# Performance work log

Hardware: AMD Instinct MI355X
Metric: run time of the kernel (lower is better)

The kernel has to match this reference:

```python
import jax, jax.numpy as jnp
import numpy as np

B, S, D = 4, 2048, 1024
H, DK, DV = 16, 64, 64
LN_EPS = 1e-5


def setup_inputs() -> dict:
    key = jax.random.key(0)
    ks = jax.random.split(key, 6)
    x = jax.random.normal(ks[0], (B, S, D), dtype=jnp.float32)
    # causal mask: True = masked position (j > i), broadcast over batch
    causal = jnp.triu(jnp.ones((S, S), dtype=bool), k=1)
    attention_mask = jnp.broadcast_to(causal, (B, S, S))
    scale = 1.0 / np.sqrt(D)
    w_q = jax.random.normal(ks[1], (D, H * DK), dtype=jnp.float32) * scale
    w_k = jax.random.normal(ks[2], (D, H * DK), dtype=jnp.float32) * scale
    w_v = jax.random.normal(ks[3], (D, H * DV), dtype=jnp.float32) * scale
    w_fc = jax.random.normal(ks[4], (H * DV, D), dtype=jnp.float32) * (1.0 / np.sqrt(H * DV))
    ln_gamma = jnp.ones((D,), dtype=jnp.float32)
    ln_beta = jnp.zeros((D,), dtype=jnp.float32)
    return {"x": x, "attention_mask": attention_mask, "w_q": w_q, "w_k": w_k,
            "w_v": w_v, "w_fc": w_fc, "ln_gamma": ln_gamma, "ln_beta": ln_beta}


def _layernorm(y, gamma, beta):
    mu = jnp.mean(y, axis=-1, keepdims=True)
    var = jnp.mean(jnp.square(y - mu), axis=-1, keepdims=True)
    return (y - mu) * jax.lax.rsqrt(var + LN_EPS) * gamma + beta


def reference(x, attention_mask, w_q, w_k, w_v, w_fc, ln_gamma, ln_beta):
    b, s, _ = x.shape
    # projections -> [b, h, s, dk/dv]
    q = (x @ w_q).reshape(b, s, H, DK).transpose(0, 2, 1, 3)
    k = (x @ w_k).reshape(b, s, H, DK).transpose(0, 2, 1, 3)
    v = (x @ w_v).reshape(b, s, H, DV).transpose(0, 2, 1, 3)
    # scaled dot-product attention with mask (True -> -1e9)
    scores = jnp.einsum('bhqd,bhkd->bhqk', q, k) / np.sqrt(DK)
    scores = jnp.where(attention_mask[:, None, :, :], jnp.float32(-1e9), scores)
    attn = jax.nn.softmax(scores, axis=-1)
    context = jnp.einsum('bhqk,bhkd->bhqd', attn, v)
    context = context.transpose(0, 2, 1, 3).reshape(b, s, H * DV)
    output = context @ w_fc
    out = _layernorm(output + x, ln_gamma, ln_beta)
    return out, attn
```

## Files before the change

### kernel.cpp

```cpp
#include <hip/hip_runtime.h>
#include <stdint.h>

#define S_LEN 2048
#define NHEAD 16

typedef short short8 __attribute__((ext_vector_type(8)));
typedef float f32x4 __attribute__((ext_vector_type(4)));
typedef unsigned short u16;

typedef __attribute__((address_space(1))) uint32_t AS1u32;
typedef __attribute__((address_space(3))) uint32_t AS3u32;

#define MFMA16(a, b, c) __builtin_amdgcn_mfma_f32_16x16x32_bf16((a), (b), (c), 0, 0, 0)

__device__ __forceinline__ void gload16(const void* g, void* l) {
  __builtin_amdgcn_global_load_lds((AS1u32*)g, (AS3u32*)l, 16, 0, 0);
}

__device__ __forceinline__ u16 f2bf(float f) {
  union { float f; uint32_t u; } c; c.f = f;
  return (u16)((c.u + 0x7fffu + ((c.u >> 16) & 1u)) >> 16);
}

__global__ __launch_bounds__(256) void prep_kernel(
    const float* __restrict__ x, u16* __restrict__ xb,
    const float* __restrict__ w0, const float* __restrict__ w1,
    const float* __restrict__ w2, const float* __restrict__ w3,
    u16* __restrict__ qkvT, u16* __restrict__ fcT) {
  __shared__ float t[32][33];
  int bid = blockIdx.x;
  if (bid < 8192) {
    size_t i = ((size_t)bid * 256 + threadIdx.x) * 4;
    f32x4 v = *(const f32x4*)(x + i);
    union { u16 h[4]; uint2 d; } o;
    o.h[0] = f2bf(v[0]); o.h[1] = f2bf(v[1]); o.h[2] = f2bf(v[2]); o.h[3] = f2bf(v[3]);
    *(uint2*)(xb + i) = o.d;
    return;
  }
  int r = bid - 8192;
  int z = r >> 10; r &= 1023;
  int bx = r & 31, by = r >> 5;
  const float* w = (z == 0) ? w0 : (z == 1) ? w1 : (z == 2) ? w2 : w3;
  u16* o = (z == 3) ? fcT : qkvT + (size_t)z * 1048576;
  float scale = (z == 0) ? 0.125f : 1.0f;
  int n0 = bx * 32, k0 = by * 32;
  int tx = threadIdx.x & 31, ty = threadIdx.x >> 5;
#pragma unroll
  for (int i = 0; i < 4; ++i) {
    int k = ty * 4 + i;
    t[k][tx] = w[(size_t)(k0 + k) * 1024 + n0 + tx];
  }
  __syncthreads();
#pragma unroll
  for (int i = 0; i < 4; ++i) {
    int n = ty * 4 + i;
    o[(size_t)(n0 + n) * 1024 + k0 + tx] = f2bf(t[tx][n] * scale);
  }
}

__device__ __forceinline__ void gemm_stage(const char* Ab, const char* Bb, u16* As, u16* Bs,
                                           int m0, int n0, int kbyte, int tid) {
#pragma unroll
  for (int i = 0; i < 2; ++i) {
    int cid = i * 256 + tid;
    int row = cid >> 2, c = cid & 3;
    int off = kbyte + ((c ^ ((row >> 1) & 3)) << 4);
    gload16(Ab + (size_t)(m0 + row) * 2048 + off, (char*)As + i * 4096 + (tid & ~63) * 16);
    gload16(Bb + (size_t)(n0 + row) * 2048 + off, (char*)Bs + i * 4096 + (tid & ~63) * 16);
  }
}

__global__ __launch_bounds__(256) void gemm_bt_kernel(
    const u16* __restrict__ A, const u16* __restrict__ BT,
    void* __restrict__ out, void* __restrict__ outv, int mode) {
  __shared__ u16 sh[128 * 128];
  u16* As = sh;
  u16* Bs = sh + 4096;
  const int tid = threadIdx.x;
  const int lane = tid & 63, wv = tid >> 6;
  const int l15 = lane & 15, h16 = lane >> 4;
  const int wr = wv >> 1, wc = wv & 1;
  const int m0 = blockIdx.x * 128, n0 = blockIdx.y * 128;
  const char* Ab = (const char*)A;
  const char* Bb = (const char*)BT;

  f32x4 acc[4][4];
#pragma unroll
  for (int i = 0; i < 4; ++i)
#pragma unroll
    for (int j = 0; j < 4; ++j) acc[i][j] = (f32x4){0.f, 0.f, 0.f, 0.f};

  gemm_stage(Ab, Bb, As, Bs, m0, n0, 0, tid);
  for (int kt = 0; kt < 32; ++kt) {
    __syncthreads();
    short8 a[4], b[4];
#pragma unroll
    for (int mf = 0; mf < 4; ++mf) {
      int row = wr * 64 + mf * 16 + l15;
      a[mf] = *(const short8*)((const char*)As + row * 64 + ((h16 ^ ((row >> 1) & 3)) << 4));
    }
#pragma unroll
    for (int nf = 0; nf < 4; ++nf) {
      int row = wc * 64 + nf * 16 + l15;
      b[nf] = *(const short8*)((const char*)Bs + row * 64 + ((h16 ^ ((row >> 1) & 3)) << 4));
    }
#pragma unroll
    for (int mf = 0; mf < 4; ++mf)
#pragma unroll
      for (int nf = 0; nf < 4; ++nf)
        acc[mf][nf] = MFMA16(a[mf], b[nf], acc[mf][nf]);
    __syncthreads();
    if (kt + 1 < 32) gemm_stage(Ab, Bb, As, Bs, m0, n0, (kt + 1) * 64, tid);
  }

  if (mode == 0 && n0 < 2048) {
    u16* o = (u16*)out;
#pragma unroll
    for (int mf = 0; mf < 4; ++mf)
#pragma unroll
      for (int nf = 0; nf < 4; ++nf)
#pragma unroll
        for (int r = 0; r < 4; ++r) {
          int row = wr * 64 + mf * 16 + 4 * h16 + r;
          int col = wc * 64 + nf * 16 + l15;
          *(u16*)((char*)sh + row * 256 + (((col >> 3) ^ (row & 7)) << 4) + (col & 7) * 2) =
              f2bf(acc[mf][nf][r]);
        }
    __syncthreads();
    int row = tid >> 1, hf = tid & 1;
    int m = m0 + row;
    int bb = m >> 11, s = m & 2047;
    int n_base = n0 + hf * 64;
    int z = n_base >> 10, nn = n_base & 1023, hh = nn >> 6;
    u16* dst = o + (size_t)z * 8388608 + (((size_t)(bb * NHEAD + hh) * S_LEN + s) << 6);
#pragma unroll
    for (int i = 0; i < 8; ++i) {
      int ch = hf * 8 + i;
      short8 v = *(const short8*)((const char*)sh + row * 256 + ((ch ^ (row & 7)) << 4));
      *(short8*)(dst + i * 8) = v;
    }
  } else if (mode == 0) {
    u16* o = (u16*)outv;
#pragma unroll
    for (int mf = 0; mf < 4; ++mf)
#pragma unroll
      for (int nf = 0; nf < 4; ++nf)
#pragma unroll
        for (int r = 0; r < 4; ++r) {
          int row = wr * 64 + mf * 16 + 4 * h16 + r;
          int col = wc * 64 + nf * 16 + l15;
          *(u16*)((char*)sh + col * 256 + (((row >> 3) ^ (col & 7)) << 4) + (row & 7) * 2) =
              f2bf(acc[mf][nf][r]);
        }
    __syncthreads();
    int col = tid >> 1, half = tid & 1;
    int bb = m0 >> 11, s0 = (m0 & 2047) + half * 64;
    int nn = n0 - 2048 + col;
    int hh = nn >> 6, dv = nn & 63;
    u16* dst = o + ((size_t)(bb * NHEAD + hh) * 64 + dv) * S_LEN + s0;
    const char* base = (const char*)sh + col * 256;
#pragma unroll
    for (int i = 0; i < 8; ++i) {
      int ch = (half * 8 + i) ^ (col & 7);
      *(short8*)(dst + i * 8) = *(const short8*)(base + (ch << 4));
    }
  } else {
    float* o = (float*)out;
#pragma unroll
    for (int mf = 0; mf < 4; ++mf)
#pragma unroll
      for (int nf = 0; nf < 4; ++nf)
#pragma unroll
        for (int r = 0; r < 4; ++r) {
          int m = m0 + wr * 64 + mf * 16 + 4 * h16 + r;
          int n = n0 + wc * 64 + nf * 16 + l15;
          o[(size_t)m * 1024 + n] = acc[mf][nf][r];
        }
  }
}

__device__ __forceinline__ void stage_qk(const char* base, int row0, u16* dst, int tid) {
#pragma unroll
  for (int i = 0; i < 2; ++i) {
    int cid = i * 512 + tid;
    int row = cid >> 3, c = cid & 7;
    gload16(base + (size_t)(row0 + row) * 128 + ((c ^ (row & 7)) << 4),
            (char*)dst + i * 8192 + (tid & ~63) * 16);
  }
}
__device__ __forceinline__ void stage_v(const char* Vb, int kv0, u16* dst, int tid) {
#pragma unroll
  for (int i = 0; i < 2; ++i) {
    int cid = i * 512 + tid;
    int row = cid >> 4, c = cid & 15;
    gload16(Vb + (size_t)row * 4096 + (size_t)kv0 * 2 + ((c ^ (row & 7)) << 4),
            (char*)dst + i * 8192 + (tid & ~63) * 16);
  }
}

__device__ __forceinline__ void qk_tile(const char* Kc, const short8* qf,
                                        f32x4* sc, int l15, int h16) {
#pragma unroll
  for (int nf = 0; nf < 8; ++nf) sc[nf] = (f32x4){0.f, 0.f, 0.f, 0.f};
#pragma unroll
  for (int ks = 0; ks < 2; ++ks)
#pragma unroll
    for (int nf = 0; nf < 8; ++nf) {
      int row = nf * 16 + l15;
      short8 kb = *(const short8*)(Kc + row * 128 + (((ks * 4 + h16) ^ (row & 7)) << 4));
      sc[nf] = MFMA16(qf[ks], kb, sc[nf]);
    }
}

__device__ __forceinline__ void attn_one(
    const u16* __restrict__ Q, const u16* __restrict__ K, const u16* __restrict__ VT,
    float* __restrict__ attn, u16* __restrict__ ctx, int qt, int bh, int tid,
    u16 (*Ks)[128 * 64], u16* Vs, u16* Ps) {
  const int lane = tid & 63, wv = tid >> 6;
  const int l15 = lane & 15, h16 = lane >> 4;
  const int w16 = wv * 16;
  const int q0 = qt * 128;
  const char* Qb = (const char*)(Q + (size_t)bh * S_LEN * 64);
  const char* Kb = (const char*)(K + (size_t)bh * S_LEN * 64);
  const char* Vb = (const char*)(VT + (size_t)bh * 64 * S_LEN);
  float* attb = attn + (size_t)bh * S_LEN * S_LEN;

  stage_qk(Qb, q0, Ps, tid);
  stage_qk(Kb, q0, Ks[0], tid);
  __syncthreads();
  short8 qf[2];
  {
    int row = w16 + l15;
    qf[0] = *(const short8*)((const char*)Ps + row * 128 + ((h16 ^ (row & 7)) << 4));
    qf[1] = *(const short8*)((const char*)Ps + row * 128 + (((4 + h16) ^ (row & 7)) << 4));
  }
  __syncthreads();

  float lsum[4] = {0.f, 0.f, 0.f, 0.f};
  int cur = 0;
  for (int t = qt; t >= 0; --t) {
    if (t > 0) stage_qk(Kb, (t - 1) * 128, Ks[cur ^ 1], tid);
    f32x4 sc[8];
    qk_tile((const char*)Ks[cur], qf, sc, l15, h16);
    if (t == qt) {
#pragma unroll
      for (int nf = 0; nf < 8; ++nf)
#pragma unroll
        for (int r = 0; r < 4; ++r)
          if (nf * 16 + l15 > w16 + 4 * h16 + r) sc[nf][r] = -1e30f;
    }
#pragma unroll
    for (int nf = 0; nf < 8; ++nf)
#pragma unroll
      for (int r = 0; r < 4; ++r) lsum[r] += __expf(sc[nf][r]);
    __syncthreads();
    cur ^= 1;
  }
  cur ^= 1;
  f32x4 ri;
#pragma unroll
  for (int r = 0; r < 4; ++r) {
    float v = lsum[r];
    v += __shfl_xor(v, 1);
    v += __shfl_xor(v, 2);
    v += __shfl_xor(v, 4);
    v += __shfl_xor(v, 8);
    ri[r] = 1.0f / v;
  }

  f32x4 cacc[4];
#pragma unroll
  for (int nf = 0; nf < 4; ++nf) cacc[nf] = (f32x4){0.f, 0.f, 0.f, 0.f};

  for (int t = 0; t <= qt; ++t) {
    const int kv0 = t * 128;
    stage_v(Vb, kv0, Vs, tid);
    f32x4 sc[8];
    qk_tile((const char*)Ks[cur], qf, sc, l15, h16);
    if (t == qt) {
#pragma unroll
      for (int nf = 0; nf < 8; ++nf)
#pragma unroll
        for (int r = 0; r < 4; ++r)
          if (nf * 16 + l15 > w16 + 4 * h16 + r) sc[nf][r] = -1e30f;
    }
    {
      float* arow = attb + (size_t)(q0 + w16 + 4 * h16) * S_LEN + kv0 + l15;
#pragma unroll
      for (int nf = 0; nf < 8; ++nf)
#pragma unroll
        for (int r = 0; r < 4; ++r) {
          float p = __expf(sc[nf][r]) * ri[r];
          int rowL = w16 + 4 * h16 + r;
          int chunk = 2 * nf + (l15 >> 3);
          *(u16*)((char*)Ps + rowL * 256 + ((chunk ^ (rowL & 7)) << 4) + (l15 & 7) * 2) = f2bf(p);
          arow[(size_t)r * S_LEN + nf * 16] = p;
        }
    }
    __syncthreads();
    if (t < qt) stage_qk(Kb, kv0 + 128, Ks[cur ^ 1], tid);
#pragma unroll
    for (int ks = 0; ks < 4; ++ks) {
      int rowP = w16 + l15;
      short8 pa = *(const short8*)((const char*)Ps + rowP * 256 + (((ks * 4 + h16) ^ (rowP & 7)) << 4));
#pragma unroll
      for (int nf = 0; nf < 4; ++nf) {
        int rowV = nf * 16 + l15;
        short8 vbf = *(const short8*)((const char*)Vs + rowV * 256 + (((ks * 4 + h16) ^ (rowV & 7)) << 4));
        cacc[nf] = MFMA16(pa, vbf, cacc[nf]);
      }
    }
    __syncthreads();
    cur ^= 1;
  }

  for (int kvt = qt + 1; kvt < 16; ++kvt) {
    const int kv0 = kvt * 128;
    int row = tid >> 2, sub = tid & 3;
    float* arow = attb + (size_t)(q0 + row) * S_LEN + kv0;
    f32x4 z = {0.f, 0.f, 0.f, 0.f};
#pragma unroll
    for (int c8 = 0; c8 < 4; ++c8) {
      int chunk = sub + 4 * c8;
      *(f32x4*)(arow + chunk * 8) = z;
      *(f32x4*)(arow + chunk * 8 + 4) = z;
    }
  }

  {
    int b = bh >> 4, hh = bh & 15;
#pragma unroll
    for (int nf = 0; nf < 4; ++nf)
#pragma unroll
      for (int r = 0; r < 4; ++r) {
        int qrow = q0 + w16 + 4 * h16 + r;
        ctx[((size_t)b * S_LEN + qrow) * 1024 + hh * 64 + nf * 16 + l15] = f2bf(cacc[nf][r]);
      }
  }
}

__global__ __launch_bounds__(512) void attn2_kernel(
    const u16* __restrict__ Q, const u16* __restrict__ K, const u16* __restrict__ VT,
    float* __restrict__ attn, u16* __restrict__ ctx) {
  __shared__ u16 Ks[2][128 * 64];
  __shared__ u16 Vs[64 * 128];
  __shared__ u16 Ps[128 * 128];
  const int tid = threadIdx.x;
  const int w = blockIdx.x;
  const int bx = (w >> 3) & 7;
  const int bh = (w & 7) + ((w >> 6) << 3);
  attn_one(Q, K, VT, attn, ctx, 15 - bx, bh, tid, Ks, Vs, Ps);
  attn_one(Q, K, VT, attn, ctx, bx, bh, tid, Ks, Vs, Ps);
}

__global__ __launch_bounds__(256) void ln_kernel(float* __restrict__ io,
                                                 const float* __restrict__ x,
                                                 const float* __restrict__ gamma,
                                                 const float* __restrict__ beta) {
  int row = blockIdx.x, tid = threadIdx.x;
  size_t base = (size_t)row * 1024 + tid * 4;
  f32x4 p = *(const f32x4*)(io + base);
  f32x4 xv = *(const f32x4*)(x + base);
  f32x4 y;
  float s1 = 0.f, s2 = 0.f;
#pragma unroll
  for (int j = 0; j < 4; ++j) {
    y[j] = p[j] + xv[j];
    s1 += y[j];
    s2 += y[j] * y[j];
  }
#pragma unroll
  for (int off = 1; off <= 32; off <<= 1) {
    s1 += __shfl_xor(s1, off);
    s2 += __shfl_xor(s2, off);
  }
  __shared__ float r1[4], r2[4];
  int w = tid >> 6;
  if ((tid & 63) == 0) { r1[w] = s1; r2[w] = s2; }
  __syncthreads();
  float S1 = r1[0] + r1[1] + r1[2] + r1[3];
  float S2 = r2[0] + r2[1] + r2[2] + r2[3];
  float mu = S1 * (1.f / 1024.f);
  float var = S2 * (1.f / 1024.f) - mu * mu;
  float rs = rsqrtf(var + 1e-5f);
  f32x4 g = *(const f32x4*)(gamma + tid * 4);
  f32x4 bt = *(const f32x4*)(beta + tid * 4);
  f32x4 o;
#pragma unroll
  for (int j = 0; j < 4; ++j) o[j] = (y[j] - mu) * rs * g[j] + bt[j];
  *(f32x4*)(io + base) = o;
}

extern "C" void kernel_launch(void* const* d_in, const int* in_sizes, int n_in,
                              void* d_out, int out_size, void* d_ws, size_t ws_size,
                              hipStream_t stream) {
  (void)in_sizes; (void)n_in; (void)out_size; (void)ws_size;
  const float* x = (const float*)d_in[0];
  const float* wq = (const float*)d_in[2];
  const float* wk = (const float*)d_in[3];
  const float* wv = (const float*)d_in[4];
  const float* wfc = (const float*)d_in[5];
  const float* gamma = (const float*)d_in[6];
  const float* beta = (const float*)d_in[7];

  char* ws = (char*)d_ws;
  u16* xb = (u16*)ws;
  u16* wqkvT = (u16*)(ws + (16u << 20));
  u16* wfcT = (u16*)(ws + (22u << 20));
  u16* qkb = (u16*)(ws + (24u << 20));
  u16* qb = qkb;
  u16* kb = qkb + (size_t)8388608;
  u16* vT = (u16*)(ws + (56u << 20));
  u16* ctx = xb;

  float* outp = (float*)d_out;
  float* attnp = outp + (size_t)4 * 2048 * 1024;

  prep_kernel<<<12288, 256, 0, stream>>>(x, xb, wq, wk, wv, wfc, wqkvT, wfcT);
  gemm_bt_kernel<<<dim3(64, 24), 256, 0, stream>>>(xb, wqkvT, qkb, vT, 0);
  attn2_kernel<<<512, 512, 0, stream>>>(qb, kb, vT, attnp, ctx);
  gemm_bt_kernel<<<dim3(64, 8), 256, 0, stream>>>(ctx, wfcT, outp, nullptr, 1);
  ln_kernel<<<8192, 256, 0, stream>>>(outp, x, gamma, beta);
}
```

Baseline: 473.1 us.

## Rewrite attention as per-wave 16-row strips with direct global loads and shuffles

Replaces the block-cooperative 128x128 attention tile, which staged K and V in shared memory behind block-wide barriers, with independent per-wavefront 16-query-row strips. Each wave loads Q, K and V fragments straight from global memory and computes 16x16 score tiles with swapped MFMA operands. It rebuilds the P operand for the PV product through cross-lane shuffles instead of an LDS round trip, and uses a small LDS transpose only to coalesce the fp32 attention stores. The intent is to remove __syncthreads stalls, improve causal load balance and raise occupancy. The cost is that K and V are no longer shared across waves, so global/L2 traffic rises, and the smaller MFMA tiles reuse less data.

```diff
diff --git a/kernel.cpp b/kernel.cpp
--- a/kernel.cpp
+++ b/kernel.cpp
@@ -179,178 +179,155 @@
   }
 }
 
-__device__ __forceinline__ void stage_qk(const char* base, int row0, u16* dst, int tid) {
-#pragma unroll
-  for (int i = 0; i < 2; ++i) {
-    int cid = i * 512 + tid;
-    int row = cid >> 3, c = cid & 7;
-    gload16(base + (size_t)(row0 + row) * 128 + ((c ^ (row & 7)) << 4),
-            (char*)dst + i * 8192 + (tid & ~63) * 16);
-  }
-}
-__device__ __forceinline__ void stage_v(const char* Vb, int kv0, u16* dst, int tid) {
-#pragma unroll
-  for (int i = 0; i < 2; ++i) {
-    int cid = i * 512 + tid;
-    int row = cid >> 4, c = cid & 15;
-    gload16(Vb + (size_t)row * 4096 + (size_t)kv0 * 2 + ((c ^ (row & 7)) << 4),
-            (char*)dst + i * 8192 + (tid & ~63) * 16);
-  }
-}
-
-__device__ __forceinline__ void qk_tile(const char* Kc, const short8* qf,
-                                        f32x4* sc, int l15, int h16) {
-#pragma unroll
-  for (int nf = 0; nf < 8; ++nf) sc[nf] = (f32x4){0.f, 0.f, 0.f, 0.f};
-#pragma unroll
-  for (int ks = 0; ks < 2; ++ks)
-#pragma unroll
-    for (int nf = 0; nf < 8; ++nf) {
-      int row = nf * 16 + l15;
-      short8 kb = *(const short8*)(Kc + row * 128 + (((ks * 4 + h16) ^ (row & 7)) << 4));
-      sc[nf] = MFMA16(qf[ks], kb, sc[nf]);
-    }
-}
-
-__device__ __forceinline__ void attn_one(
-    const u16* __restrict__ Q, const u16* __restrict__ K, const u16* __restrict__ VT,
-    float* __restrict__ attn, u16* __restrict__ ctx, int qt, int bh, int tid,
-    u16 (*Ks)[128 * 64], u16* Vs, u16* Ps) {
-  const int lane = tid & 63, wv = tid >> 6;
+__device__ __forceinline__ void attn3_strip(
+    const u16* __restrict__ Qb, const u16* __restrict__ Kb, const u16* __restrict__ Vb,
+    float* __restrict__ attb, u16* __restrict__ ctx, int bh, int s, int lane,
+    float (*myP)[20]) {
   const int l15 = lane & 15, h16 = lane >> 4;
-  const int w16 = wv * 16;
-  const int q0 = qt * 128;
-  const char* Qb = (const char*)(Q + (size_t)bh * S_LEN * 64);
-  const char* Kb = (const char*)(K + (size_t)bh * S_LEN * 64);
-  const char* Vb = (const char*)(VT + (size_t)bh * 64 * S_LEN);
-  float* attb = attn + (size_t)bh * S_LEN * S_LEN;
-
-  stage_qk(Qb, q0, Ps, tid);
-  stage_qk(Kb, q0, Ks[0], tid);
-  __syncthreads();
-  short8 qf[2];
-  {
-    int row = w16 + l15;
-    qf[0] = *(const short8*)((const char*)Ps + row * 128 + ((h16 ^ (row & 7)) << 4));
-    qf[1] = *(const short8*)((const char*)Ps + row * 128 + (((4 + h16) ^ (row & 7)) << 4));
-  }
-  __syncthreads();
-
-  float lsum[4] = {0.f, 0.f, 0.f, 0.f};
-  int cur = 0;
-  for (int t = qt; t >= 0; --t) {
-    if (t > 0) stage_qk(Kb, (t - 1) * 128, Ks[cur ^ 1], tid);
-    f32x4 sc[8];
-    qk_tile((const char*)Ks[cur], qf, sc, l15, h16);
-    if (t == qt) {
-#pragma unroll
-      for (int nf = 0; nf < 8; ++nf)
+  const int q0 = s * 16;
+  const u16* qrow = Qb + (size_t)(q0 + l15) * 64 + h16 * 8;
+  const short8 qf0 = *(const short8*)qrow;
+  const short8 qf1 = *(const short8*)(qrow + 32);
+  const u16* kbase = Kb + (size_t)l15 * 64 + h16 * 8;
+
+  float lsum = 0.f;
+  for (int t = 0; t <= s; ++t) {
+    const u16* krow = kbase + (size_t)t * 1024;
+    short8 kf0 = *(const short8*)krow;
+    short8 kf1 = *(const short8*)(krow + 32);
+    f32x4 sc = {0.f, 0.f, 0.f, 0.f};
+    sc = MFMA16(kf0, qf0, sc);
+    sc = MFMA16(kf1, qf1, sc);
+    if (t == s) {
+#pragma unroll
+      for (int r = 0; r < 4; ++r)
+        if (4 * h16 + r > l15) sc[r] = -1e30f;
+    }
+#pragma unroll
+    for (int r = 0; r < 4; ++r) lsum += __expf(sc[r]);
+  }
+  lsum += __shfl_xor(lsum, 16);
+  lsum += __shfl_xor(lsum, 32);
+  const float ri = 1.0f / lsum;
+
+  f32x4 acc[4];
+#pragma unroll
+  for (int i = 0; i < 4; ++i) acc[i] = (f32x4){0.f, 0.f, 0.f, 0.f};
+  const int qr = lane >> 2, c4 = (lane & 3) * 4;
+
+  for (int t = 0; t <= s; t += 2) {
+    uint32_t pkA0, pkA1, pkB0, pkB1;
+    {
+      const u16* krow = kbase + (size_t)t * 1024;
+      short8 kf0 = *(const short8*)krow;
+      short8 kf1 = *(const short8*)(krow + 32);
+      f32x4 sc = {0.f, 0.f, 0.f, 0.f};
+      sc = MFMA16(kf0, qf0, sc);
+      sc = MFMA16(kf1, qf1, sc);
+      if (t == s) {
 #pragma unroll
         for (int r = 0; r < 4; ++r)
-          if (nf * 16 + l15 > w16 + 4 * h16 + r) sc[nf][r] = -1e30f;
-    }
-#pragma unroll
-    for (int nf = 0; nf < 8; ++nf)
-#pragma unroll
-      for (int r = 0; r < 4; ++r) lsum[r] += __expf(sc[nf][r]);
-    __syncthreads();
-    cur ^= 1;
-  }
-  cur ^= 1;
-  f32x4 ri;
-#pragma unroll
-  for (int r = 0; r < 4; ++r) {
-    float v = lsum[r];
-    v += __shfl_xor(v, 1);
-    v += __shfl_xor(v, 2);
-    v += __shfl_xor(v, 4);
-    v += __shfl_xor(v, 8);
-    ri[r] = 1.0f / v;
-  }
-
-  f32x4 cacc[4];
-#pragma unroll
-  for (int nf = 0; nf < 4; ++nf) cacc[nf] = (f32x4){0.f, 0.f, 0.f, 0.f};
-
-  for (int t = 0; t <= qt; ++t) {
-    const int kv0 = t * 128;
-    stage_v(Vb, kv0, Vs, tid);
-    f32x4 sc[8];
-    qk_tile((const char*)Ks[cur], qf, sc, l15, h16);
-    if (t == qt) {
-#pragma unroll
-      for (int nf = 0; nf < 8; ++nf)
+          if (4 * h16 + r > l15) sc[r] = -1e30f;
+      }
+      f32x4 pr;
+#pragma unroll
+      for (int r = 0; r < 4; ++r) pr[r] = __expf(sc[r]) * ri;
+#pragma unroll
+      for (int r = 0; r < 4; ++r) myP[l15][4 * h16 + r] = pr[r];
+      pkA0 = (uint32_t)f2bf(pr[0]) | ((uint32_t)f2bf(pr[1]) << 16);
+      pkA1 = (uint32_t)f2bf(pr[2]) | ((uint32_t)f2bf(pr[3]) << 16);
+      asm volatile("s_waitcnt lgkmcnt(0)" ::: "memory");
+      f32x4 v = *(const f32x4*)&myP[qr][c4];
+      *(f32x4*)(attb + (size_t)(q0 + qr) * S_LEN + t * 16 + c4) = v;
+    }
+    if (t + 1 <= s) {
+      const u16* krow = kbase + (size_t)(t + 1) * 1024;
+      short8 kf0 = *(const short8*)krow;
+      short8 kf1 = *(const short8*)(krow + 32);
+      f32x4 sc = {0.f, 0.f, 0.f, 0.f};
+      sc = MFMA16(kf0, qf0, sc);
+      sc = MFMA16(kf1, qf1, sc);
+      if (t + 1 == s) {
 #pragma unroll
         for (int r = 0; r < 4; ++r)
-          if (nf * 16 + l15 > w16 + 4 * h16 + r) sc[nf][r] = -1e30f;
-    }
-    {
-      float* arow = attb + (size_t)(q0 + w16 + 4 * h16) * S_LEN + kv0 + l15;
-#pragma unroll
-      for (int nf = 0; nf < 8; ++nf)
-#pragma unroll
-        for (int r = 0; r < 4; ++r) {
-          float p = __expf(sc[nf][r]) * ri[r];
-          int rowL = w16 + 4 * h16 + r;
-          int chunk = 2 * nf + (l15 >> 3);
-          *(u16*)((char*)Ps + rowL * 256 + ((chunk ^ (rowL & 7)) << 4) + (l15 & 7) * 2) = f2bf(p);
-          arow[(size_t)r * S_LEN + nf * 16] = p;
-        }
-    }
-    __syncthreads();
-    if (t < qt) stage_qk(Kb, kv0 + 128, Ks[cur ^ 1], tid);
-#pragma unroll
-    for (int ks = 0; ks < 4; ++ks) {
-      int rowP = w16 + l15;
-      short8 pa = *(const short8*)((const char*)Ps + rowP * 256 + (((ks * 4 + h16) ^ (rowP & 7)) << 4));
-#pragma unroll
-      for (int nf = 0; nf < 4; ++nf) {
-        int rowV = nf * 16 + l15;
-        short8 vbf = *(const short8*)((const char*)Vs + rowV * 256 + (((ks * 4 + h16) ^ (rowV & 7)) << 4));
-        cacc[nf] = MFMA16(pa, vbf, cacc[nf]);
+          if (4 * h16 + r > l15) sc[r] = -1e30f;
       }
-    }
-    __syncthreads();
-    cur ^= 1;
-  }
-
-  for (int kvt = qt + 1; kvt < 16; ++kvt) {
-    const int kv0 = kvt * 128;
-    int row = tid >> 2, sub = tid & 3;
-    float* arow = attb + (size_t)(q0 + row) * S_LEN + kv0;
-    f32x4 z = {0.f, 0.f, 0.f, 0.f};
-#pragma unroll
-    for (int c8 = 0; c8 < 4; ++c8) {
-      int chunk = sub + 4 * c8;
-      *(f32x4*)(arow + chunk * 8) = z;
-      *(f32x4*)(arow + chunk * 8 + 4) = z;
+      f32x4 pr;
+#pragma unroll
+      for (int r = 0; r < 4; ++r) pr[r] = __expf(sc[r]) * ri;
+#pragma unroll
+      for (int r = 0; r < 4; ++r) myP[l15][4 * h16 + r] = pr[r];
+      pkB0 = (uint32_t)f2bf(pr[0]) | ((uint32_t)f2bf(pr[1]) << 16);
+      pkB1 = (uint32_t)f2bf(pr[2]) | ((uint32_t)f2bf(pr[3]) << 16);
+      asm volatile("s_waitcnt lgkmcnt(0)" ::: "memory");
+      f32x4 v = *(const f32x4*)&myP[qr][c4];
+      *(f32x4*)(attb + (size_t)(q0 + qr) * S_LEN + (t + 1) * 16 + c4) = v;
+    } else {
+      pkB0 = 0; pkB1 = 0;
+    }
+    int lo = ((h16 & 1) << 5) + l15;
+    int hi = lo + 16;
+    uint32_t a0 = (uint32_t)__shfl((int)pkA0, lo);
+    uint32_t a1 = (uint32_t)__shfl((int)pkA1, lo);
+    uint32_t a2 = (uint32_t)__shfl((int)pkA0, hi);
+    uint32_t a3 = (uint32_t)__shfl((int)pkA1, hi);
+    uint32_t b0 = (uint32_t)__shfl((int)pkB0, lo);
+    uint32_t b1 = (uint32_t)__shfl((int)pkB1, lo);
+    uint32_t b2 = (uint32_t)__shfl((int)pkB0, hi);
+    uint32_t b3 = (uint32_t)__shfl((int)pkB1, hi);
+    union { uint32_t u[4]; short8 s8; } pf;
+    bool tB = (h16 >= 2);
+    pf.u[0] = tB ? b0 : a0;
+    pf.u[1] = tB ? b1 : a1;
+    pf.u[2] = tB ? b2 : a2;
+    pf.u[3] = tB ? b3 : a3;
+#pragma unroll
+    for (int dvt = 0; dvt < 4; ++dvt) {
+      const u16* vrow = Vb + (size_t)(dvt * 16 + l15) * S_LEN + t * 16 + h16 * 8;
+      short8 vf = *(const short8*)vrow;
+      acc[dvt] = MFMA16(vf, pf.s8, acc[dvt]);
     }
   }
 
   {
     int b = bh >> 4, hh = bh & 15;
-#pragma unroll
-    for (int nf = 0; nf < 4; ++nf)
-#pragma unroll
-      for (int r = 0; r < 4; ++r) {
-        int qrow = q0 + w16 + 4 * h16 + r;
-        ctx[((size_t)b * S_LEN + qrow) * 1024 + hh * 64 + nf * 16 + l15] = f2bf(cacc[nf][r]);
-      }
-  }
-}
-
-__global__ __launch_bounds__(512) void attn2_kernel(
+    u16* crow = ctx + ((size_t)b * S_LEN + q0 + l15) * 1024 + hh * 64;
+#pragma unroll
+    for (int dvt = 0; dvt < 4; ++dvt)
+#pragma unroll
+      for (int r = 0; r < 4; ++r)
+        crow[dvt * 16 + 4 * h16 + r] = f2bf(acc[dvt][r]);
+  }
+
+  {
+    int start = (s + 1) * 16;
+    int a64 = (start + 63) & ~63;
+    if (a64 > S_LEN) a64 = S_LEN;
+    f32x4 z = {0.f, 0.f, 0.f, 0.f};
+    for (int kv0 = start; kv0 < a64; kv0 += 16)
+      *(f32x4*)(attb + (size_t)(q0 + l15) * S_LEN + kv0 + h16 * 4) = z;
+    for (int kv0 = a64; kv0 < S_LEN; kv0 += 64) {
+#pragma unroll
+      for (int g = 0; g < 4; ++g)
+        *(f32x4*)(attb + (size_t)(q0 + g * 4 + h16) * S_LEN + kv0 + l15 * 4) = z;
+    }
+  }
+}
+
+__global__ __launch_bounds__(512, 4) void attn3_kernel(
     const u16* __restrict__ Q, const u16* __restrict__ K, const u16* __restrict__ VT,
     float* __restrict__ attn, u16* __restrict__ ctx) {
-  __shared__ u16 Ks[2][128 * 64];
-  __shared__ u16 Vs[64 * 128];
-  __shared__ u16 Ps[128 * 128];
-  const int tid = threadIdx.x;
+  __shared__ float ldsP[8][16][20];
+  const int tid = threadIdx.x, wv = tid >> 6, lane = tid & 63;
   const int w = blockIdx.x;
-  const int bx = (w >> 3) & 7;
   const int bh = (w & 7) + ((w >> 6) << 3);
-  attn_one(Q, K, VT, attn, ctx, 15 - bx, bh, tid, Ks, Vs, Ps);
-  attn_one(Q, K, VT, attn, ctx, bx, bh, tid, Ks, Vs, Ps);
+  const int p = ((w >> 3) & 7) * 8 + wv;
+  const u16* Qb = Q + (size_t)bh * S_LEN * 64;
+  const u16* Kb = K + (size_t)bh * S_LEN * 64;
+  const u16* Vb = VT + (size_t)bh * 64 * S_LEN;
+  float* attb = attn + (size_t)bh * S_LEN * S_LEN;
+  attn3_strip(Qb, Kb, Vb, attb, ctx, bh, 127 - p, lane, ldsP[wv]);
+  attn3_strip(Qb, Kb, Vb, attb, ctx, bh, p, lane, ldsP[wv]);
 }
 
 __global__ __launch_bounds__(256) void ln_kernel(float* __restrict__ io,
@@ -418,7 +395,7 @@
 
   prep_kernel<<<12288, 256, 0, stream>>>(x, xb, wq, wk, wv, wfc, wqkvT, wfcT);
   gemm_bt_kernel<<<dim3(64, 24), 256, 0, stream>>>(xb, wqkvT, qkb, vT, 0);
-  attn2_kernel<<<512, 512, 0, stream>>>(qb, kb, vT, attnp, ctx);
+  attn3_kernel<<<512, 512, 0, stream>>>(qb, kb, vT, attnp, ctx);
   gemm_bt_kernel<<<dim3(64, 8), 256, 0, stream>>>(ctx, wfcT, outp, nullptr, 1);
   ln_kernel<<<8192, 256, 0, stream>>>(outp, x, gamma, beta);
 }
```

New measurement: 744.3 us. +57.3%, slower.

## Shrink attention query/key tiles to 64 with 256-thread blocks and 1024 workgroups

Applied to the files above, without the earlier changes.

The attention kernel moves from 128-row query/key tiles with 512-thread blocks to 64-row tiles with 256-thread blocks, launching 1024 workgroups that each handle a paired heavy and light causal tile. Shared memory per block drops from about 64KB to 24KB, which should allow more resident blocks per CU and better load balance on the causal triangle. Masked-region waste on the diagonal tile also shrinks. In exchange there are twice as many loop iterations and barriers per unit of work, and each MFMA tile does less work per K/V load, which lowers data reuse.

```diff
diff --git a/kernel.cpp b/kernel.cpp
--- a/kernel.cpp
+++ b/kernel.cpp
@@ -179,54 +179,63 @@
   }
 }
 
-__device__ __forceinline__ void stage_qk(const char* base, int row0, u16* dst, int tid) {
+__device__ __forceinline__ void stage_q64(const char* Qb, int q0, u16* dst, int tid) {
 #pragma unroll
   for (int i = 0; i < 2; ++i) {
-    int cid = i * 512 + tid;
+    int cid = i * 256 + tid;
     int row = cid >> 3, c = cid & 7;
-    gload16(base + (size_t)(row0 + row) * 128 + ((c ^ (row & 7)) << 4),
-            (char*)dst + i * 8192 + (tid & ~63) * 16);
-  }
-}
-__device__ __forceinline__ void stage_v(const char* Vb, int kv0, u16* dst, int tid) {
+    gload16(Qb + (size_t)(q0 + row) * 128 + ((c ^ (row & 7)) << 4),
+            (char*)dst + i * 4096 + (tid & ~63) * 16);
+  }
+}
+__device__ __forceinline__ void stage_k64(const char* Kb, int kv0, u16* dst, int tid) {
 #pragma unroll
   for (int i = 0; i < 2; ++i) {
-    int cid = i * 512 + tid;
-    int row = cid >> 4, c = cid & 15;
+    int cid = i * 256 + tid;
+    int row = cid >> 3, c = cid & 7;
+    gload16(Kb + (size_t)(kv0 + row) * 128 + ((c ^ (row & 7)) << 4),
+            (char*)dst + i * 4096 + (tid & ~63) * 16);
+  }
+}
+__device__ __forceinline__ void stage_v64(const char* Vb, int kv0, u16* dst, int tid) {
+#pragma unroll
+  for (int i = 0; i < 2; ++i) {
+    int cid = i * 256 + tid;
+    int row = cid >> 3, c = cid & 7;
     gload16(Vb + (size_t)row * 4096 + (size_t)kv0 * 2 + ((c ^ (row & 7)) << 4),
-            (char*)dst + i * 8192 + (tid & ~63) * 16);
-  }
-}
-
-__device__ __forceinline__ void qk_tile(const char* Kc, const short8* qf,
-                                        f32x4* sc, int l15, int h16) {
-#pragma unroll
-  for (int nf = 0; nf < 8; ++nf) sc[nf] = (f32x4){0.f, 0.f, 0.f, 0.f};
+            (char*)dst + i * 4096 + (tid & ~63) * 16);
+  }
+}
+
+__device__ __forceinline__ void qk_tile64(const char* Kc, const short8* qf,
+                                          f32x4* sc, int l15, int h16) {
+#pragma unroll
+  for (int nf = 0; nf < 4; ++nf) sc[nf] = (f32x4){0.f, 0.f, 0.f, 0.f};
 #pragma unroll
   for (int ks = 0; ks < 2; ++ks)
 #pragma unroll
-    for (int nf = 0; nf < 8; ++nf) {
+    for (int nf = 0; nf < 4; ++nf) {
       int row = nf * 16 + l15;
       short8 kb = *(const short8*)(Kc + row * 128 + (((ks * 4 + h16) ^ (row & 7)) << 4));
       sc[nf] = MFMA16(qf[ks], kb, sc[nf]);
     }
 }
 
-__device__ __forceinline__ void attn_one(
+__device__ __forceinline__ void attn4_one(
     const u16* __restrict__ Q, const u16* __restrict__ K, const u16* __restrict__ VT,
-    float* __restrict__ attn, u16* __restrict__ ctx, int qt, int bh, int tid,
-    u16 (*Ks)[128 * 64], u16* Vs, u16* Ps) {
+    float* __restrict__ attn, u16* __restrict__ ctx, int s, int bh, int tid,
+    u16 (*Ks)[64 * 64], u16* Vs, u16* Ps) {
   const int lane = tid & 63, wv = tid >> 6;
   const int l15 = lane & 15, h16 = lane >> 4;
   const int w16 = wv * 16;
-  const int q0 = qt * 128;
+  const int q0 = s * 64;
   const char* Qb = (const char*)(Q + (size_t)bh * S_LEN * 64);
   const char* Kb = (const char*)(K + (size_t)bh * S_LEN * 64);
   const char* Vb = (const char*)(VT + (size_t)bh * 64 * S_LEN);
   float* attb = attn + (size_t)bh * S_LEN * S_LEN;
 
-  stage_qk(Qb, q0, Ps, tid);
-  stage_qk(Kb, q0, Ks[0], tid);
+  stage_q64(Qb, q0, Ps, tid);
+  stage_k64(Kb, s * 64, Ks[0], tid);
   __syncthreads();
   short8 qf[2];
   {
@@ -238,19 +247,19 @@
 
   float lsum[4] = {0.f, 0.f, 0.f, 0.f};
   int cur = 0;
-  for (int t = qt; t >= 0; --t) {
-    if (t > 0) stage_qk(Kb, (t - 1) * 128, Ks[cur ^ 1], tid);
-    f32x4 sc[8];
-    qk_tile((const char*)Ks[cur], qf, sc, l15, h16);
-    if (t == qt) {
-#pragma unroll
-      for (int nf = 0; nf < 8; ++nf)
+  for (int t = s; t >= 0; --t) {
+    if (t > 0) stage_k64(Kb, (t - 1) * 64, Ks[cur ^ 1], tid);
+    f32x4 sc[4];
+    qk_tile64((const char*)Ks[cur], qf, sc, l15, h16);
+    if (t == s) {
+#pragma unroll
+      for (int nf = 0; nf < 4; ++nf)
 #pragma unroll
         for (int r = 0; r < 4; ++r)
           if (nf * 16 + l15 > w16 + 4 * h16 + r) sc[nf][r] = -1e30f;
     }
 #pragma unroll
-    for (int nf = 0; nf < 8; ++nf)
+    for (int nf = 0; nf < 4; ++nf)
 #pragma unroll
       for (int r = 0; r < 4; ++r) lsum[r] += __expf(sc[nf][r]);
     __syncthreads();
@@ -272,14 +281,14 @@
 #pragma unroll
   for (int nf = 0; nf < 4; ++nf) cacc[nf] = (f32x4){0.f, 0.f, 0.f, 0.f};
 
-  for (int t = 0; t <= qt; ++t) {
-    const int kv0 = t * 128;
-    stage_v(Vb, kv0, Vs, tid);
-    f32x4 sc[8];
-    qk_tile((const char*)Ks[cur], qf, sc, l15, h16);
-    if (t == qt) {
-#pragma unroll
-      for (int nf = 0; nf < 8; ++nf)
+  for (int t = 0; t <= s; ++t) {
+    const int kv0 = t * 64;
+    stage_v64(Vb, kv0, Vs, tid);
+    f32x4 sc[4];
+    qk_tile64((const char*)Ks[cur], qf, sc, l15, h16);
+    if (t == s) {
+#pragma unroll
+      for (int nf = 0; nf < 4; ++nf)
 #pragma unroll
         for (int r = 0; r < 4; ++r)
           if (nf * 16 + l15 > w16 + 4 * h16 + r) sc[nf][r] = -1e30f;
@@ -287,26 +296,26 @@
     {
       float* arow = attb + (size_t)(q0 + w16 + 4 * h16) * S_LEN + kv0 + l15;
 #pragma unroll
-      for (int nf = 0; nf < 8; ++nf)
+      for (int nf = 0; nf < 4; ++nf)
 #pragma unroll
         for (int r = 0; r < 4; ++r) {
           float p = __expf(sc[nf][r]) * ri[r];
           int rowL = w16 + 4 * h16 + r;
           int chunk = 2 * nf + (l15 >> 3);
-          *(u16*)((char*)Ps + rowL * 256 + ((chunk ^ (rowL & 7)) << 4) + (l15 & 7) * 2) = f2bf(p);
+          *(u16*)((char*)Ps + rowL * 128 + ((chunk ^ (rowL & 7)) << 4) + (l15 & 7) * 2) = f2bf(p);
           arow[(size_t)r * S_LEN + nf * 16] = p;
         }
     }
     __syncthreads();
-    if (t < qt) stage_qk(Kb, kv0 + 128, Ks[cur ^ 1], tid);
-#pragma unroll
-    for (int ks = 0; ks < 4; ++ks) {
+    if (t < s) stage_k64(Kb, kv0 + 64, Ks[cur ^ 1], tid);
+#pragma unroll
+    for (int ks = 0; ks < 2; ++ks) {
       int rowP = w16 + l15;
-      short8 pa = *(const short8*)((const char*)Ps + rowP * 256 + (((ks * 4 + h16) ^ (rowP & 7)) << 4));
+      short8 pa = *(const short8*)((const char*)Ps + rowP * 128 + (((ks * 4 + h16) ^ (rowP & 7)) << 4));
 #pragma unroll
       for (int nf = 0; nf < 4; ++nf) {
         int rowV = nf * 16 + l15;
-        short8 vbf = *(const short8*)((const char*)Vs + rowV * 256 + (((ks * 4 + h16) ^ (rowV & 7)) << 4));
+        short8 vbf = *(const short8*)((const char*)Vs + rowV * 128 + (((ks * 4 + h16) ^ (rowV & 7)) << 4));
         cacc[nf] = MFMA16(pa, vbf, cacc[nf]);
       }
     }
@@ -314,16 +323,14 @@
     cur ^= 1;
   }
 
-  for (int kvt = qt + 1; kvt < 16; ++kvt) {
-    const int kv0 = kvt * 128;
+  {
     int row = tid >> 2, sub = tid & 3;
-    float* arow = attb + (size_t)(q0 + row) * S_LEN + kv0;
     f32x4 z = {0.f, 0.f, 0.f, 0.f};
-#pragma unroll
-    for (int c8 = 0; c8 < 4; ++c8) {
-      int chunk = sub + 4 * c8;
-      *(f32x4*)(arow + chunk * 8) = z;
-      *(f32x4*)(arow + chunk * 8 + 4) = z;
+    for (int kv0 = (s + 1) * 64; kv0 < S_LEN; kv0 += 64) {
+      float* arow = attb + (size_t)(q0 + row) * S_LEN + kv0;
+#pragma unroll
+      for (int c8 = 0; c8 < 4; ++c8)
+        *(f32x4*)(arow + (sub + 4 * c8) * 4) = z;
     }
   }
 
@@ -339,18 +346,18 @@
   }
 }
 
-__global__ __launch_bounds__(512) void attn2_kernel(
+__global__ __launch_bounds__(256) void attn4_kernel(
     const u16* __restrict__ Q, const u16* __restrict__ K, const u16* __restrict__ VT,
     float* __restrict__ attn, u16* __restrict__ ctx) {
-  __shared__ u16 Ks[2][128 * 64];
-  __shared__ u16 Vs[64 * 128];
-  __shared__ u16 Ps[128 * 128];
+  __shared__ u16 Ks[2][64 * 64];
+  __shared__ u16 Vs[64 * 64];
+  __shared__ u16 Ps[64 * 64];
   const int tid = threadIdx.x;
   const int w = blockIdx.x;
-  const int bx = (w >> 3) & 7;
-  const int bh = (w & 7) + ((w >> 6) << 3);
-  attn_one(Q, K, VT, attn, ctx, 15 - bx, bh, tid, Ks, Vs, Ps);
-  attn_one(Q, K, VT, attn, ctx, bx, bh, tid, Ks, Vs, Ps);
+  const int bx = (w >> 3) & 15;
+  const int bh = (w & 7) | ((w >> 7) << 3);
+  attn4_one(Q, K, VT, attn, ctx, 31 - bx, bh, tid, Ks, Vs, Ps);
+  attn4_one(Q, K, VT, attn, ctx, bx, bh, tid, Ks, Vs, Ps);
 }
 
 __global__ __launch_bounds__(256) void ln_kernel(float* __restrict__ io,
@@ -418,7 +425,7 @@
 
   prep_kernel<<<12288, 256, 0, stream>>>(x, xb, wq, wk, wv, wfc, wqkvT, wfcT);
   gemm_bt_kernel<<<dim3(64, 24), 256, 0, stream>>>(xb, wqkvT, qkb, vT, 0);
-  attn2_kernel<<<512, 512, 0, stream>>>(qb, kb, vT, attnp, ctx);
+  attn4_kernel<<<1024, 256, 0, stream>>>(qb, kb, vT, attnp, ctx);
   gemm_bt_kernel<<<dim3(64, 8), 256, 0, stream>>>(ctx, wfcT, outp, nullptr, 1);
   ln_kernel<<<8192, 256, 0, stream>>>(outp, x, gamma, beta);
 }
```

After: 513.3 us. 8.5% more time.

## Transpose QK MFMA to keep P in registers and drop LDS P buffer

Applied to the files above, without the earlier changes.

Swaps the MFMA operand order so each lane holds four consecutive key columns of one query row. The attention probabilities can then be written as 16-byte vector stores. The bf16 P fragment is rebuilt for the PV MFMA with cross-lane shuffles instead of a round trip through a 32KB shared-memory buffer, and Q is loaded straight from global memory. Removing the P buffer cuts LDS use, which should allow higher occupancy (launch bounds now request 6 waves per EU) and removes scattered 2-byte LDS writes. The cost is many shuffle instructions per k-step and scattered 2-byte context stores.

```diff
diff --git a/kernel.cpp b/kernel.cpp
--- a/kernel.cpp
+++ b/kernel.cpp
@@ -198,116 +198,109 @@
   }
 }
 
-__device__ __forceinline__ void qk_tile(const char* Kc, const short8* qf,
-                                        f32x4* sc, int l15, int h16) {
-#pragma unroll
-  for (int nf = 0; nf < 8; ++nf) sc[nf] = (f32x4){0.f, 0.f, 0.f, 0.f};
-#pragma unroll
-  for (int ks = 0; ks < 2; ++ks)
-#pragma unroll
-    for (int nf = 0; nf < 8; ++nf) {
-      int row = nf * 16 + l15;
-      short8 kb = *(const short8*)(Kc + row * 128 + (((ks * 4 + h16) ^ (row & 7)) << 4));
-      sc[nf] = MFMA16(qf[ks], kb, sc[nf]);
-    }
-}
-
-__device__ __forceinline__ void attn_one(
+__device__ __forceinline__ void attn5_one(
     const u16* __restrict__ Q, const u16* __restrict__ K, const u16* __restrict__ VT,
     float* __restrict__ attn, u16* __restrict__ ctx, int qt, int bh, int tid,
-    u16 (*Ks)[128 * 64], u16* Vs, u16* Ps) {
+    u16 (*Ks)[128 * 64], u16* Vs) {
   const int lane = tid & 63, wv = tid >> 6;
   const int l15 = lane & 15, h16 = lane >> 4;
   const int w16 = wv * 16;
   const int q0 = qt * 128;
-  const char* Qb = (const char*)(Q + (size_t)bh * S_LEN * 64);
   const char* Kb = (const char*)(K + (size_t)bh * S_LEN * 64);
   const char* Vb = (const char*)(VT + (size_t)bh * 64 * S_LEN);
   float* attb = attn + (size_t)bh * S_LEN * S_LEN;
 
-  stage_qk(Qb, q0, Ps, tid);
+  const u16* qrow = Q + (size_t)bh * S_LEN * 64 + (size_t)(q0 + w16 + l15) * 64 + h16 * 8;
+  const short8 qf0 = *(const short8*)qrow;
+  const short8 qf1 = *(const short8*)(qrow + 32);
+
   stage_qk(Kb, q0, Ks[0], tid);
   __syncthreads();
-  short8 qf[2];
-  {
-    int row = w16 + l15;
-    qf[0] = *(const short8*)((const char*)Ps + row * 128 + ((h16 ^ (row & 7)) << 4));
-    qf[1] = *(const short8*)((const char*)Ps + row * 128 + (((4 + h16) ^ (row & 7)) << 4));
-  }
-  __syncthreads();
-
-  float lsum[4] = {0.f, 0.f, 0.f, 0.f};
+
+  float lsum = 0.f;
   int cur = 0;
   for (int t = qt; t >= 0; --t) {
     if (t > 0) stage_qk(Kb, (t - 1) * 128, Ks[cur ^ 1], tid);
-    f32x4 sc[8];
-    qk_tile((const char*)Ks[cur], qf, sc, l15, h16);
-    if (t == qt) {
-#pragma unroll
-      for (int nf = 0; nf < 8; ++nf)
+    const char* Kc = (const char*)Ks[cur];
+#pragma unroll
+    for (int nf = 0; nf < 8; ++nf) {
+      int row = nf * 16 + l15;
+      short8 k0 = *(const short8*)(Kc + row * 128 + ((h16 ^ (row & 7)) << 4));
+      short8 k1 = *(const short8*)(Kc + row * 128 + (((4 + h16) ^ (row & 7)) << 4));
+      f32x4 sc = {0.f, 0.f, 0.f, 0.f};
+      sc = MFMA16(k0, qf0, sc);
+      sc = MFMA16(k1, qf1, sc);
+      if (t == qt) {
 #pragma unroll
         for (int r = 0; r < 4; ++r)
-          if (nf * 16 + l15 > w16 + 4 * h16 + r) sc[nf][r] = -1e30f;
-    }
-#pragma unroll
-    for (int nf = 0; nf < 8; ++nf)
-#pragma unroll
-      for (int r = 0; r < 4; ++r) lsum[r] += __expf(sc[nf][r]);
+          if (nf * 16 + 4 * h16 + r > w16 + l15) sc[r] = -1e30f;
+      }
+#pragma unroll
+      for (int r = 0; r < 4; ++r) lsum += __expf(sc[r]);
+    }
     __syncthreads();
     cur ^= 1;
   }
   cur ^= 1;
-  f32x4 ri;
-#pragma unroll
-  for (int r = 0; r < 4; ++r) {
-    float v = lsum[r];
-    v += __shfl_xor(v, 1);
-    v += __shfl_xor(v, 2);
-    v += __shfl_xor(v, 4);
-    v += __shfl_xor(v, 8);
-    ri[r] = 1.0f / v;
-  }
-
-  f32x4 cacc[4];
-#pragma unroll
-  for (int nf = 0; nf < 4; ++nf) cacc[nf] = (f32x4){0.f, 0.f, 0.f, 0.f};
+  lsum += __shfl_xor(lsum, 16);
+  lsum += __shfl_xor(lsum, 32);
+  const float ri = 1.0f / lsum;
+
+  f32x4 acc[4];
+#pragma unroll
+  for (int i = 0; i < 4; ++i) acc[i] = (f32x4){0.f, 0.f, 0.f, 0.f};
 
   for (int t = 0; t <= qt; ++t) {
     const int kv0 = t * 128;
     stage_v(Vb, kv0, Vs, tid);
-    f32x4 sc[8];
-    qk_tile((const char*)Ks[cur], qf, sc, l15, h16);
-    if (t == qt) {
-#pragma unroll
-      for (int nf = 0; nf < 8; ++nf)
+    const char* Kc = (const char*)Ks[cur];
+    uint32_t pk[16];
+    float* arow = attb + (size_t)(q0 + w16 + l15) * S_LEN + kv0 + 4 * h16;
+#pragma unroll
+    for (int nf = 0; nf < 8; ++nf) {
+      int row = nf * 16 + l15;
+      short8 k0 = *(const short8*)(Kc + row * 128 + ((h16 ^ (row & 7)) << 4));
+      short8 k1 = *(const short8*)(Kc + row * 128 + (((4 + h16) ^ (row & 7)) << 4));
+      f32x4 sc = {0.f, 0.f, 0.f, 0.f};
+      sc = MFMA16(k0, qf0, sc);
+      sc = MFMA16(k1, qf1, sc);
+      if (t == qt) {
 #pragma unroll
         for (int r = 0; r < 4; ++r)
-          if (nf * 16 + l15 > w16 + 4 * h16 + r) sc[nf][r] = -1e30f;
-    }
-    {
-      float* arow = attb + (size_t)(q0 + w16 + 4 * h16) * S_LEN + kv0 + l15;
-#pragma unroll
-      for (int nf = 0; nf < 8; ++nf)
-#pragma unroll
-        for (int r = 0; r < 4; ++r) {
-          float p = __expf(sc[nf][r]) * ri[r];
-          int rowL = w16 + 4 * h16 + r;
-          int chunk = 2 * nf + (l15 >> 3);
-          *(u16*)((char*)Ps + rowL * 256 + ((chunk ^ (rowL & 7)) << 4) + (l15 & 7) * 2) = f2bf(p);
-          arow[(size_t)r * S_LEN + nf * 16] = p;
-        }
+          if (nf * 16 + 4 * h16 + r > w16 + l15) sc[r] = -1e30f;
+      }
+      f32x4 pr;
+#pragma unroll
+      for (int r = 0; r < 4; ++r) pr[r] = __expf(sc[r]) * ri;
+      *(f32x4*)(arow + nf * 16) = pr;
+      pk[2 * nf] = (uint32_t)f2bf(pr[0]) | ((uint32_t)f2bf(pr[1]) << 16);
+      pk[2 * nf + 1] = (uint32_t)f2bf(pr[2]) | ((uint32_t)f2bf(pr[3]) << 16);
     }
     __syncthreads();
     if (t < qt) stage_qk(Kb, kv0 + 128, Ks[cur ^ 1], tid);
+    const int lo = ((h16 & 1) << 5) + l15;
+    const int hi = lo + 16;
+    const bool tB = (h16 >= 2);
 #pragma unroll
     for (int ks = 0; ks < 4; ++ks) {
-      int rowP = w16 + l15;
-      short8 pa = *(const short8*)((const char*)Ps + rowP * 256 + (((ks * 4 + h16) ^ (rowP & 7)) << 4));
-#pragma unroll
-      for (int nf = 0; nf < 4; ++nf) {
-        int rowV = nf * 16 + l15;
-        short8 vbf = *(const short8*)((const char*)Vs + rowV * 256 + (((ks * 4 + h16) ^ (rowV & 7)) << 4));
-        cacc[nf] = MFMA16(pa, vbf, cacc[nf]);
+      uint32_t a0 = (uint32_t)__shfl((int)pk[4 * ks + 0], lo);
+      uint32_t a1 = (uint32_t)__shfl((int)pk[4 * ks + 1], lo);
+      uint32_t a2 = (uint32_t)__shfl((int)pk[4 * ks + 0], hi);
+      uint32_t a3 = (uint32_t)__shfl((int)pk[4 * ks + 1], hi);
+      uint32_t b0 = (uint32_t)__shfl((int)pk[4 * ks + 2], lo);
+      uint32_t b1 = (uint32_t)__shfl((int)pk[4 * ks + 3], lo);
+      uint32_t b2 = (uint32_t)__shfl((int)pk[4 * ks + 2], hi);
+      uint32_t b3 = (uint32_t)__shfl((int)pk[4 * ks + 3], hi);
+      union { uint32_t u[4]; short8 s8; } pf;
+      pf.u[0] = tB ? b0 : a0;
+      pf.u[1] = tB ? b1 : a1;
+      pf.u[2] = tB ? b2 : a2;
+      pf.u[3] = tB ? b3 : a3;
+#pragma unroll
+      for (int dvt = 0; dvt < 4; ++dvt) {
+        int rowV = dvt * 16 + l15;
+        short8 vf = *(const short8*)((const char*)Vs + rowV * 256 + (((ks * 4 + h16) ^ (rowV & 7)) << 4));
+        acc[dvt] = MFMA16(vf, pf.s8, acc[dvt]);
       }
     }
     __syncthreads();
@@ -317,40 +310,38 @@
   for (int kvt = qt + 1; kvt < 16; ++kvt) {
     const int kv0 = kvt * 128;
     int row = tid >> 2, sub = tid & 3;
-    float* arow = attb + (size_t)(q0 + row) * S_LEN + kv0;
+    float* az = attb + (size_t)(q0 + row) * S_LEN + kv0;
     f32x4 z = {0.f, 0.f, 0.f, 0.f};
 #pragma unroll
     for (int c8 = 0; c8 < 4; ++c8) {
       int chunk = sub + 4 * c8;
-      *(f32x4*)(arow + chunk * 8) = z;
-      *(f32x4*)(arow + chunk * 8 + 4) = z;
+      *(f32x4*)(az + chunk * 8) = z;
+      *(f32x4*)(az + chunk * 8 + 4) = z;
     }
   }
 
   {
     int b = bh >> 4, hh = bh & 15;
-#pragma unroll
-    for (int nf = 0; nf < 4; ++nf)
-#pragma unroll
-      for (int r = 0; r < 4; ++r) {
-        int qrow = q0 + w16 + 4 * h16 + r;
-        ctx[((size_t)b * S_LEN + qrow) * 1024 + hh * 64 + nf * 16 + l15] = f2bf(cacc[nf][r]);
-      }
-  }
-}
-
-__global__ __launch_bounds__(512) void attn2_kernel(
+    u16* crow = ctx + ((size_t)b * S_LEN + q0 + w16 + l15) * 1024 + hh * 64;
+#pragma unroll
+    for (int dvt = 0; dvt < 4; ++dvt)
+#pragma unroll
+      for (int r = 0; r < 4; ++r)
+        crow[dvt * 16 + 4 * h16 + r] = f2bf(acc[dvt][r]);
+  }
+}
+
+__global__ __launch_bounds__(512, 6) void attn5_kernel(
     const u16* __restrict__ Q, const u16* __restrict__ K, const u16* __restrict__ VT,
     float* __restrict__ attn, u16* __restrict__ ctx) {
   __shared__ u16 Ks[2][128 * 64];
   __shared__ u16 Vs[64 * 128];
-  __shared__ u16 Ps[128 * 128];
   const int tid = threadIdx.x;
   const int w = blockIdx.x;
   const int bx = (w >> 3) & 7;
   const int bh = (w & 7) + ((w >> 6) << 3);
-  attn_one(Q, K, VT, attn, ctx, 15 - bx, bh, tid, Ks, Vs, Ps);
-  attn_one(Q, K, VT, attn, ctx, bx, bh, tid, Ks, Vs, Ps);
+  attn5_one(Q, K, VT, attn, ctx, 15 - bx, bh, tid, Ks, Vs);
+  attn5_one(Q, K, VT, attn, ctx, bx, bh, tid, Ks, Vs);
 }
 
 __global__ __launch_bounds__(256) void ln_kernel(float* __restrict__ io,
@@ -418,7 +409,7 @@
 
   prep_kernel<<<12288, 256, 0, stream>>>(x, xb, wq, wk, wv, wfc, wqkvT, wfcT);
   gemm_bt_kernel<<<dim3(64, 24), 256, 0, stream>>>(xb, wqkvT, qkb, vT, 0);
-  attn2_kernel<<<512, 512, 0, stream>>>(qb, kb, vT, attnp, ctx);
+  attn5_kernel<<<512, 512, 0, stream>>>(qb, kb, vT, attnp, ctx);
   gemm_bt_kernel<<<dim3(64, 8), 256, 0, stream>>>(ctx, wfcT, outp, nullptr, 1);
   ln_kernel<<<8192, 256, 0, stream>>>(outp, x, gamma, beta);
 }
```

New measurement: 547.0 us. +15.6%, slower.
